# Optimization experiments

Hardware: AMD Instinct MI355X
Metric: run time of the kernel (lower is better)

## Reference

```python
import jax, jax.numpy as jnp
import numpy as np

BITS = 2
GROUP_SIZE = 128
EPS = 1e-8


def fake_quant(w):
    """Per-group (contiguous 128-element, over flattened weight) min/max fake quantization."""
    max_q = (1 << BITS) - 1  # 3 for INT2
    flat = w.reshape(-1, GROUP_SIZE)            # [num_groups, group_size]
    mn = flat.min(axis=1, keepdims=True)
    mx = flat.max(axis=1, keepdims=True)
    rng = mx - mn
    scale = rng / max_q
    safe_scale = jnp.where(rng < EPS, 1.0, scale)  # avoid div-by-zero
    q = jnp.clip(jnp.round((flat - mn) / safe_scale), 0, max_q)
    deq = q * scale + mn
    out = jnp.where(rng < EPS, flat, deq)        # pass-through for near-constant groups
    return out.reshape(w.shape)


def setup_inputs() -> dict:
    key = jax.random.key(0)
    kx, kw, kb = jax.random.split(key, 3)
    B, S, D_IN, D_OUT = 4, 2048, 4096, 4096
    x = jax.random.normal(kx, (B, S, D_IN), dtype=jnp.float32)
    # kaiming-uniform-like init scale
    bound = float(np.sqrt(6.0 / D_IN))
    weight = jax.random.uniform(kw, (D_OUT, D_IN), minval=-bound, maxval=bound, dtype=jnp.float32)
    bias = jnp.zeros((D_OUT,), dtype=jnp.float32)
    return {"x": x, "weight": weight, "bias": bias}


def reference(x, weight, bias):
    # training-mode forward: STE fake-quant of weight, then linear
    w_quant = weight + jax.lax.stop_gradient(fake_quant(weight) - weight)
    return jnp.einsum('bsd,od->bso', x, w_quant) + bias
```

## Files before the change

### kernel.cpp

```cpp
#include <hip/hip_runtime.h>
#include <hip/hip_bf16.h>
#include <stdint.h>

#define M_DIM 8192
#define N_DIM 4096
#define K_DIM 4096

typedef __hip_bfloat16 bf16;
typedef __attribute__((ext_vector_type(8))) short bf16x8;
typedef __attribute__((ext_vector_type(4))) float floatx4;

__device__ __forceinline__ uint2 pack_bf16x4(float4 v) {
  bf16 b0 = __float2bfloat16(v.x);
  bf16 b1 = __float2bfloat16(v.y);
  bf16 b2 = __float2bfloat16(v.z);
  bf16 b3 = __float2bfloat16(v.w);
  unsigned int lo = (unsigned int)*(unsigned short*)&b0 |
                    ((unsigned int)*(unsigned short*)&b1 << 16);
  unsigned int hi = (unsigned int)*(unsigned short*)&b2 |
                    ((unsigned int)*(unsigned short*)&b3 << 16);
  return make_uint2(lo, hi);
}

__global__ void quant_w_kernel(const float* __restrict__ w, bf16* __restrict__ wq) {
  const int t = blockIdx.x * blockDim.x + threadIdx.x;
  const int g = t >> 4;
  const int s = t & 15;

  const float4* p = (const float4*)(w + (size_t)g * 128);
  float4 a = p[s];
  float4 b = p[s + 16];

  float mn = fminf(fminf(fminf(a.x, a.y), fminf(a.z, a.w)),
                   fminf(fminf(b.x, b.y), fminf(b.z, b.w)));
  float mx = fmaxf(fmaxf(fmaxf(a.x, a.y), fmaxf(a.z, a.w)),
                   fmaxf(fmaxf(b.x, b.y), fmaxf(b.z, b.w)));
#pragma unroll
  for (int off = 8; off >= 1; off >>= 1) {
    mn = fminf(mn, __shfl_xor(mn, off));
    mx = fmaxf(mx, __shfl_xor(mx, off));
  }
  const float rng = mx - mn;
  float4 oa, ob;
  if (rng < 1e-8f) {
    oa = a; ob = b;
  } else {
    const float scale = rng / 3.0f;
    float q0 = fminf(fmaxf(rintf((a.x - mn) / scale), 0.f), 3.f);
    float q1 = fminf(fmaxf(rintf((a.y - mn) / scale), 0.f), 3.f);
    float q2 = fminf(fmaxf(rintf((a.z - mn) / scale), 0.f), 3.f);
    float q3 = fminf(fmaxf(rintf((a.w - mn) / scale), 0.f), 3.f);
    float q4 = fminf(fmaxf(rintf((b.x - mn) / scale), 0.f), 3.f);
    float q5 = fminf(fmaxf(rintf((b.y - mn) / scale), 0.f), 3.f);
    float q6 = fminf(fmaxf(rintf((b.z - mn) / scale), 0.f), 3.f);
    float q7 = fminf(fmaxf(rintf((b.w - mn) / scale), 0.f), 3.f);
    oa = make_float4(q0 * scale + mn, q1 * scale + mn, q2 * scale + mn, q3 * scale + mn);
    ob = make_float4(q4 * scale + mn, q5 * scale + mn, q6 * scale + mn, q7 * scale + mn);
  }
  uint2* q = (uint2*)(wq + (size_t)g * 128);
  q[s]      = pack_bf16x4(oa);
  q[s + 16] = pack_bf16x4(ob);
}

__global__ void cast_x_kernel(const float* __restrict__ x, bf16* __restrict__ xb) {
  const size_t base = (size_t)blockIdx.x * 512;
  const int tid = threadIdx.x;
  const float4* p = (const float4*)x + base;
  float4 a = p[tid];
  float4 b = p[tid + 256];
  uint2* q = (uint2*)xb + base;
  q[tid]       = pack_bf16x4(a);
  q[tid + 256] = pack_bf16x4(b);
}

#define BM 128
#define BN 128
#define BK 64

typedef const uint32_t GQ __attribute__((address_space(1)));
typedef uint32_t LQ __attribute__((address_space(3)));

__global__ void gemm_bt_kernel(const bf16* __restrict__ A,
                               const bf16* __restrict__ Bw,
                               const float* __restrict__ bias,
                               float* __restrict__ C) {
  __shared__ bf16 sA[BM * BK];
  __shared__ bf16 sB[BN * BK];

  const int tid  = threadIdx.x;
  const int lane = tid & 63;
  const int warp = tid >> 6;
  const int wm   = warp & 1;
  const int wn   = warp >> 1;
  const int m0   = blockIdx.y * BM;
  const int n0   = blockIdx.x * BN;

  floatx4 acc[4][4];
#pragma unroll
  for (int i = 0; i < 4; ++i)
#pragma unroll
    for (int j = 0; j < 4; ++j)
      acc[i][j] = (floatx4){0.f, 0.f, 0.f, 0.f};

  const int srow = warp * 8 + (lane >> 3);
  const int scol = (lane & 7) * 8;

  const int fr  = lane & 15;
  const int fk  = (lane >> 4) * 8;

  for (int k0 = 0; k0 < K_DIM; k0 += BK) {
#pragma unroll
    for (int j = 0; j < 4; ++j) {
      const int r = j * 32 + srow;
      const bf16* g = A + (size_t)(m0 + r) * K_DIM + (k0 + scol);
      bf16* l = sA + (j * 32 + warp * 8) * BK;
      __builtin_amdgcn_global_load_lds((GQ*)g, (LQ*)l, 16, 0, 0);
    }
#pragma unroll
    for (int j = 0; j < 4; ++j) {
      const int r = j * 32 + srow;
      const bf16* g = Bw + (size_t)(n0 + r) * K_DIM + (k0 + scol);
      bf16* l = sB + (j * 32 + warp * 8) * BK;
      __builtin_amdgcn_global_load_lds((GQ*)g, (LQ*)l, 16, 0, 0);
    }
    __syncthreads();

#pragma unroll
    for (int kk = 0; kk < BK; kk += 32) {
      bf16x8 af[4], bfr[4];
#pragma unroll
      for (int i = 0; i < 4; ++i)
        af[i] = *(const bf16x8*)&sA[(wm * 64 + i * 16 + fr) * BK + kk + fk];
#pragma unroll
      for (int j = 0; j < 4; ++j)
        bfr[j] = *(const bf16x8*)&sB[(wn * 64 + j * 16 + fr) * BK + kk + fk];
#pragma unroll
      for (int i = 0; i < 4; ++i)
#pragma unroll
        for (int j = 0; j < 4; ++j)
          acc[i][j] = __builtin_amdgcn_mfma_f32_16x16x32_bf16(af[i], bfr[j], acc[i][j], 0, 0, 0);
    }
    __syncthreads();
  }

  const int cm = (lane >> 4) * 4;
  const int cn = lane & 15;
#pragma unroll
  for (int j = 0; j < 4; ++j) {
    const int col = n0 + wn * 64 + j * 16 + cn;
    const float bv = bias[col];
#pragma unroll
    for (int i = 0; i < 4; ++i) {
      const int rowb = m0 + wm * 64 + i * 16 + cm;
      float* out = C + (size_t)rowb * N_DIM + col;
#pragma unroll
      for (int r = 0; r < 4; ++r)
        out[(size_t)r * N_DIM] = acc[i][j][r] + bv;
    }
  }
}

extern "C" void kernel_launch(void* const* d_in, const int* in_sizes, int n_in,
                              void* d_out, int out_size, void* d_ws, size_t ws_size,
                              hipStream_t stream) {
  const float* x      = (const float*)d_in[0];
  const float* weight = (const float*)d_in[1];
  const float* bias   = (const float*)d_in[2];
  float* out          = (float*)d_out;

  bf16* wq = (bf16*)d_ws;
  bf16* xb = (bf16*)((char*)d_ws + (size_t)N_DIM * K_DIM * sizeof(bf16));

  {
    int threads = (N_DIM * K_DIM) / 8;
    quant_w_kernel<<<threads / 256, 256, 0, stream>>>(weight, wq);
  }
  {
    int threads = (M_DIM * K_DIM) / 8;
    cast_x_kernel<<<threads / 256, 256, 0, stream>>>(x, xb);
  }
  {
    dim3 grid(N_DIM / BN, M_DIM / BM);
    gemm_bt_kernel<<<grid, 256, 0, stream>>>(xb, wq, bias, out);
  }
}
```

Baseline: 539.1 us.

## Fuse preprocessing kernels and remap GEMM tiles to XCD-local N strips

Merges the activation cast and weight fake-quant into one launch, dispatching on block index. It also replaces the 2D GEMM grid with a 1D grid whose index mapping assigns each XCD (round-robin block dispatch) a contiguous strip of N tiles across all M tiles. The aim is better L2 locality for weight tiles per chiplet and less launch overhead. The change in tile ordering may alter activation reuse patterns.

```diff
diff --git a/kernel.cpp b/kernel.cpp
--- a/kernel.cpp
+++ b/kernel.cpp
@@ -22,55 +22,59 @@
   return make_uint2(lo, hi);
 }
 
-__global__ void quant_w_kernel(const float* __restrict__ w, bf16* __restrict__ wq) {
-  const int t = blockIdx.x * blockDim.x + threadIdx.x;
-  const int g = t >> 4;
-  const int s = t & 15;
+#define CAST_BLOCKS ((M_DIM * K_DIM) / 8 / 256)
+#define QUANT_BLOCKS ((N_DIM * K_DIM) / 8 / 256)
 
-  const float4* p = (const float4*)(w + (size_t)g * 128);
-  float4 a = p[s];
-  float4 b = p[s + 16];
+__global__ void aux_kernel(const float* __restrict__ x, bf16* __restrict__ xb,
+                           const float* __restrict__ w, bf16* __restrict__ wq) {
+  if (blockIdx.x < CAST_BLOCKS) {
+    const size_t base = (size_t)blockIdx.x * 512;
+    const int tid = threadIdx.x;
+    const float4* p = (const float4*)x + base;
+    float4 a = p[tid];
+    float4 b = p[tid + 256];
+    uint2* q = (uint2*)xb + base;
+    q[tid]       = pack_bf16x4(a);
+    q[tid + 256] = pack_bf16x4(b);
+  } else {
+    const int t = (blockIdx.x - CAST_BLOCKS) * blockDim.x + threadIdx.x;
+    const int g = t >> 4;
+    const int s = t & 15;
 
-  float mn = fminf(fminf(fminf(a.x, a.y), fminf(a.z, a.w)),
-                   fminf(fminf(b.x, b.y), fminf(b.z, b.w)));
-  float mx = fmaxf(fmaxf(fmaxf(a.x, a.y), fmaxf(a.z, a.w)),
-                   fmaxf(fmaxf(b.x, b.y), fmaxf(b.z, b.w)));
+    const float4* p = (const float4*)(w + (size_t)g * 128);
+    float4 a = p[s];
+    float4 b = p[s + 16];
+
+    float mn = fminf(fminf(fminf(a.x, a.y), fminf(a.z, a.w)),
+                     fminf(fminf(b.x, b.y), fminf(b.z, b.w)));
+    float mx = fmaxf(fmaxf(fmaxf(a.x, a.y), fmaxf(a.z, a.w)),
+                     fmaxf(fmaxf(b.x, b.y), fmaxf(b.z, b.w)));
 #pragma unroll
-  for (int off = 8; off >= 1; off >>= 1) {
-    mn = fminf(mn, __shfl_xor(mn, off));
-    mx = fmaxf(mx, __shfl_xor(mx, off));
+    for (int off = 8; off >= 1; off >>= 1) {
+      mn = fminf(mn, __shfl_xor(mn, off));
+      mx = fmaxf(mx, __shfl_xor(mx, off));
+    }
+    const float rng = mx - mn;
+    float4 oa, ob;
+    if (rng < 1e-8f) {
+      oa = a; ob = b;
+    } else {
+      const float scale = rng / 3.0f;
+      float q0 = fminf(fmaxf(rintf((a.x - mn) / scale), 0.f), 3.f);
+      float q1 = fminf(fmaxf(rintf((a.y - mn) / scale), 0.f), 3.f);
+      float q2 = fminf(fmaxf(rintf((a.z - mn) / scale), 0.f), 3.f);
+      float q3 = fminf(fmaxf(rintf((a.w - mn) / scale), 0.f), 3.f);
+      float q4 = fminf(fmaxf(rintf((b.x - mn) / scale), 0.f), 3.f);
+      float q5 = fminf(fmaxf(rintf((b.y - mn) / scale), 0.f), 3.f);
+      float q6 = fminf(fmaxf(rintf((b.z - mn) / scale), 0.f), 3.f);
+      float q7 = fminf(fmaxf(rintf((b.w - mn) / scale), 0.f), 3.f);
+      oa = make_float4(q0 * scale + mn, q1 * scale + mn, q2 * scale + mn, q3 * scale + mn);
+      ob = make_float4(q4 * scale + mn, q5 * scale + mn, q6 * scale + mn, q7 * scale + mn);
+    }
+    uint2* q = (uint2*)(wq + (size_t)g * 128);
+    q[s]      = pack_bf16x4(oa);
+    q[s + 16] = pack_bf16x4(ob);
   }
-  const float rng = mx - mn;
-  float4 oa, ob;
-  if (rng < 1e-8f) {
-    oa = a; ob = b;
-  } else {
-    const float scale = rng / 3.0f;
-    float q0 = fminf(fmaxf(rintf((a.x - mn) / scale), 0.f), 3.f);
-    float q1 = fminf(fmaxf(rintf((a.y - mn) / scale), 0.f), 3.f);
-    float q2 = fminf(fmaxf(rintf((a.z - mn) / scale), 0.f), 3.f);
-    float q3 = fminf(fmaxf(rintf((a.w - mn) / scale), 0.f), 3.f);
-    float q4 = fminf(fmaxf(rintf((b.x - mn) / scale), 0.f), 3.f);
-    float q5 = fminf(fmaxf(rintf((b.y - mn) / scale), 0.f), 3.f);
-    float q6 = fminf(fmaxf(rintf((b.z - mn) / scale), 0.f), 3.f);
-    float q7 = fminf(fmaxf(rintf((b.w - mn) / scale), 0.f), 3.f);
-    oa = make_float4(q0 * scale + mn, q1 * scale + mn, q2 * scale + mn, q3 * scale + mn);
-    ob = make_float4(q4 * scale + mn, q5 * scale + mn, q6 * scale + mn, q7 * scale + mn);
-  }
-  uint2* q = (uint2*)(wq + (size_t)g * 128);
-  q[s]      = pack_bf16x4(oa);
-  q[s + 16] = pack_bf16x4(ob);
-}
-
-__global__ void cast_x_kernel(const float* __restrict__ x, bf16* __restrict__ xb) {
-  const size_t base = (size_t)blockIdx.x * 512;
-  const int tid = threadIdx.x;
-  const float4* p = (const float4*)x + base;
-  float4 a = p[tid];
-  float4 b = p[tid + 256];
-  uint2* q = (uint2*)xb + base;
-  q[tid]       = pack_bf16x4(a);
-  q[tid + 256] = pack_bf16x4(b);
 }
 
 #define BM 128
@@ -92,8 +96,14 @@
   const int warp = tid >> 6;
   const int wm   = warp & 1;
   const int wn   = warp >> 1;
-  const int m0   = blockIdx.y * BM;
-  const int n0   = blockIdx.x * BN;
+
+  const int linear = blockIdx.x;
+  const int strip  = linear & 7;
+  const int within = linear >> 3;
+  const int mt     = within & 63;
+  const int nsub   = within >> 6;
+  const int m0     = mt * BM;
+  const int n0     = (strip * 4 + nsub) * BN;
 
   floatx4 acc[4][4];
 #pragma unroll
@@ -171,16 +181,7 @@
   bf16* wq = (bf16*)d_ws;
   bf16* xb = (bf16*)((char*)d_ws + (size_t)N_DIM * K_DIM * sizeof(bf16));
 
-  {
-    int threads = (N_DIM * K_DIM) / 8;
-    quant_w_kernel<<<threads / 256, 256, 0, stream>>>(weight, wq);
-  }
-  {
-    int threads = (M_DIM * K_DIM) / 8;
-    cast_x_kernel<<<threads / 256, 256, 0, stream>>>(x, xb);
-  }
-  {
-    dim3 grid(N_DIM / BN, M_DIM / BM);
-    gemm_bt_kernel<<<grid, 256, 0, stream>>>(xb, wq, bias, out);
-  }
+  aux_kernel<<<CAST_BLOCKS + QUANT_BLOCKS, 256, 0, stream>>>(x, xb, weight, wq);
+
+  gemm_bt_kernel<<<(M_DIM / BM) * (N_DIM / BN), 256, 0, stream>>>(xb, wq, bias, out);
 }
```

Measured after the change: 584.4 us. 8.4% more time.
